# Optimization experiments

Measured on AMD Instinct MI355X. Metric: run time of the kernel, lower is better.

## Reference

```python
import jax, jax.numpy as jnp
import numpy as np

B, S, HIDDEN = 1, 2048, 3584
NH, NKV, HD = 16, 8, 256
N_REP = NH // NKV
EPS = 1e-6
SCALING = 256.0 ** -0.5  # query_pre_attn_scalar=256
SOFTCAP = 50.0
NEG = -1e9


def rmsnorm(x, w):
    # Gemma RMSNorm with unit offset, computed in fp32
    xf = x.astype(jnp.float32)
    n = xf * jax.lax.rsqrt(jnp.mean(xf * xf, axis=-1, keepdims=True) + EPS)
    return (n * (1.0 + w.astype(jnp.float32))).astype(x.dtype)


def rope(x, cos, sin):
    # x: [B,S,H,D]; gemma pairs (x[:D/2], x[D/2:]) as complex (rotate-half)
    x1, x2 = jnp.split(x, 2, axis=-1)
    c = cos[None, :, None, :]
    s = sin[None, :, None, :]
    return jnp.concatenate([x1 * c - x2 * s, x1 * s + x2 * c], axis=-1).astype(x.dtype)


def setup_inputs() -> dict:
    key = jax.random.key(0)
    ks = jax.random.split(key, 6)
    hidden_states = jax.random.normal(ks[0], (B, S, HIDDEN), jnp.float32)
    w_qkv = jax.random.normal(ks[1], ((NH + 2 * NKV) * HD, HIDDEN), jnp.float32) * 0.02
    w_o = jax.random.normal(ks[2], (HIDDEN, NH * HD), jnp.float32) * 0.02
    q_norm_w = jax.random.normal(ks[3], (HD,), jnp.float32) * 0.1
    k_norm_w = jax.random.normal(ks[4], (HD,), jnp.float32) * 0.1
    k_cache = jnp.zeros((B, S, NKV, HD), jnp.float32)
    v_cache = jnp.zeros((B, S, NKV, HD), jnp.float32)
    kv_write_indices = jnp.arange(S, dtype=jnp.int32)
    # rotary tables, theta=10000
    inv_freq = 1.0 / (10000.0 ** (np.arange(0, HD, 2, dtype=np.float32) / HD))
    t = np.arange(S, dtype=np.float32)
    freqs = np.outer(t, inv_freq)  # [S, HD/2]
    cos = jnp.asarray(np.cos(freqs), jnp.float32)
    sin = jnp.asarray(np.sin(freqs), jnp.float32)
    # causal additive mask [1,1,S,S]
    causal = np.tril(np.ones((S, S), dtype=bool))
    mask = jnp.asarray(np.where(causal, 0.0, NEG).astype(np.float32))[None, None]
    return {"hidden_states": hidden_states, "cos": cos, "sin": sin,
            "kv_write_indices": kv_write_indices, "k_cache": k_cache,
            "v_cache": v_cache, "mask": mask, "w_qkv": w_qkv, "w_o": w_o,
            "q_norm_w": q_norm_w, "k_norm_w": k_norm_w}


def reference(hidden_states, cos, sin, kv_write_indices, k_cache, v_cache,
              mask, w_qkv, w_o, q_norm_w, k_norm_w):
    qkv = jnp.einsum('bsh,oh->bso', hidden_states, w_qkv)
    q_size, kv_size = NH * HD, NKV * HD
    xq = qkv[..., :q_size].reshape(B, S, NH, HD)
    xk = qkv[..., q_size:q_size + kv_size].reshape(B, S, NKV, HD)
    xv = qkv[..., q_size + kv_size:].reshape(B, S, NKV, HD)
    xq = rmsnorm(xq, q_norm_w)
    xk = rmsnorm(xk, k_norm_w)
    xq = rope(xq, cos, sin)
    xk = rope(xk, cos, sin)
    # KV cache write (index_copy_ along dim 1)
    kc = k_cache.at[:, kv_write_indices].set(xk)
    vc = v_cache.at[:, kv_write_indices].set(xv)
    # GQA expand
    key = jnp.repeat(kc, N_REP, axis=2)   # [B,S,NH,HD]
    val = jnp.repeat(vc, N_REP, axis=2)
    q = xq.transpose(0, 2, 1, 3) * SCALING  # [B,NH,S,HD]
    k = key.transpose(0, 2, 1, 3)
    v = val.transpose(0, 2, 1, 3)
    scores = jnp.einsum('bhqd,bhkd->bhqk', q, k)
    scores = jnp.tanh(scores / SOFTCAP) * SOFTCAP  # logit softcapping
    scores = scores + mask
    p = jax.nn.softmax(scores, axis=-1)
    out = jnp.einsum('bhqk,bhkd->bhqd', p, v)
    out = out.transpose(0, 2, 1, 3).reshape(B, S, NH * HD)
    return jnp.einsum('bsd,hd->bsh', out, w_o)
```

## Files before the change

kernel.cpp:

```cpp
#include <hip/hip_runtime.h>

typedef __bf16 bf16;
typedef __bf16 bf16x4 __attribute__((ext_vector_type(4)));
typedef __bf16 bf16x8 __attribute__((ext_vector_type(8)));
typedef float f32x4 __attribute__((ext_vector_type(4)));

#define S_LEN 2048
#define HID   3584
#define NHEADS 16
#define NKVH   8
#define HDIM   256
#define QKV_O  8192
#define O_IN   4096

typedef const __attribute__((address_space(1))) void* gp_t;
typedef __attribute__((address_space(3))) void* sp_t;

__device__ __forceinline__ void async16(const void* g, void* s) {
  __builtin_amdgcn_global_load_lds((gp_t)g, (sp_t)s, 16, 0, 0);
}

__device__ __forceinline__ f32x4 mfma16(bf16x8 a, bf16x8 b, f32x4 c) {
  return __builtin_amdgcn_mfma_f32_16x16x32_bf16(a, b, c, 0, 0, 0);
}

__global__ __launch_bounds__(256) void cast_kernel(const float* __restrict__ in,
                                                   bf16* __restrict__ out, int n4) {
  int i = blockIdx.x * 256 + threadIdx.x;
  if (i >= n4) return;
  f32x4 v = ((const f32x4*)in)[i];
  bf16x4 o = { (bf16)v[0], (bf16)v[1], (bf16)v[2], (bf16)v[3] };
  ((bf16x4*)out)[i] = o;
}

__global__ __launch_bounds__(512, 2) void gemm_nt_8p(const bf16* __restrict__ A,
                                                     const bf16* __restrict__ B,
                                                     float* __restrict__ C,
                                                     int M, int N, int K) {
  __shared__ bf16 As0[256 * 64];
  __shared__ bf16 Bs0[256 * 64];
  __shared__ bf16 As1[256 * 64];
  __shared__ bf16 Bs1[256 * 64];
  int tid = threadIdx.x;
  int lane = tid & 63;
  int w = tid >> 6;
  int wm = w >> 2, wn = w & 3;
  int lid = blockIdx.x;
  int oid = (lid & 7) * 32 + (lid >> 3);
  int rect = oid >> 5, ri = oid & 31;
  int bm = (rect & 3) * 2 + (ri >> 4);
  int bn = (rect >> 2) * 16 + (ri & 15);
  int srow = tid >> 3, schunk = tid & 7;
  int gcol = (schunk ^ (srow & 7)) * 8;
  const bf16* Ag = A + (size_t)(bm * 256 + srow) * K + gcol;
  const bf16* Bg = B + (size_t)(bn * 256 + srow) * K + gcol;
  int soff = srow * 64 + schunk * 8;
  int fr = lane & 15, fq = lane >> 4;
  int c0 = ((fq) ^ (fr & 7)) * 8;
  int c1 = ((4 + fq) ^ (fr & 7)) * 8;
  const int arow = (wm * 128 + fr) * 64;
  const int brow = (wn * 64 + fr) * 64;

  f32x4 acc[8][4];
#pragma unroll
  for (int i = 0; i < 8; i++)
#pragma unroll
    for (int j = 0; j < 4; j++) { f32x4 z = {0.f, 0.f, 0.f, 0.f}; acc[i][j] = z; }
  bf16x8 a[8], b[8];

#define STG(gb, lb, kk, half) do {                                    \
    const bf16* _g = (gb) + (size_t)((half) * 128) * K + (kk);        \
    bf16* _l = (lb) + (half) * 128 * 64 + soff;                       \
    async16(_g, _l);                                                  \
    async16(_g + (size_t)64 * K, _l + 64 * 64);                       \
  } while (0)
#define LDA8(base, mg) do {                                           \
    const bf16* _p = (base) + arow + (mg) * 64 * 64;                  \
    _Pragma("unroll")                                                 \
    for (int i = 0; i < 4; i++) {                                     \
      a[i * 2 + 0] = *(const bf16x8*)(_p + i * 16 * 64 + c0);         \
      a[i * 2 + 1] = *(const bf16x8*)(_p + i * 16 * 64 + c1);         \
    }                                                                 \
  } while (0)
#define LDB4(base, jh) do {                                           \
    const bf16* _p = (base) + brow + (jh) * 32 * 64;                  \
    _Pragma("unroll")                                                 \
    for (int j = 0; j < 2; j++) {                                     \
      b[(jh) * 4 + j * 2 + 0] = *(const bf16x8*)(_p + j * 16 * 64 + c0); \
      b[(jh) * 4 + j * 2 + 1] = *(const bf16x8*)(_p + j * 16 * 64 + c1); \
    }                                                                 \
  } while (0)
#define MM16(mg, jh) do {                                             \
    __builtin_amdgcn_s_setprio(1);                                    \
    _Pragma("unroll")                                                 \
    for (int i = 0; i < 4; i++) {                                     \
      acc[(mg) * 4 + i][(jh) * 2 + 0] = mfma16(a[i * 2 + 0], b[(jh) * 4 + 0], acc[(mg) * 4 + i][(jh) * 2 + 0]); \
      acc[(mg) * 4 + i][(jh) * 2 + 0] = mfma16(a[i * 2 + 1], b[(jh) * 4 + 1], acc[(mg) * 4 + i][(jh) * 2 + 0]); \
      acc[(mg) * 4 + i][(jh) * 2 + 1] = mfma16(a[i * 2 + 0], b[(jh) * 4 + 2], acc[(mg) * 4 + i][(jh) * 2 + 1]); \
      acc[(mg) * 4 + i][(jh) * 2 + 1] = mfma16(a[i * 2 + 1], b[(jh) * 4 + 3], acc[(mg) * 4 + i][(jh) * 2 + 1]); \
    }                                                                 \
    __builtin_amdgcn_s_setprio(0);                                    \
  } while (0)
#define BAR() __builtin_amdgcn_s_barrier()
#define SBZ() __builtin_amdgcn_sched_barrier(0)
#define WAITV4() asm volatile("s_waitcnt vmcnt(4)" ::: "memory")

  const int nT = K >> 6;
  const int nIter = K >> 7;
  STG(Ag, As0, 0, 0); STG(Ag, As0, 0, 1);
  STG(Bg, Bs0, 0, 0); STG(Bg, Bs0, 0, 1);
  STG(Bg, Bs1, 64, 0); STG(Bg, Bs1, 64, 1);
  WAITV4();
  BAR(); SBZ();

  for (int t = 0; t < nIter; t++) {
    int T = 2 * t;
    int kA1 = (T + 1) * 64;
    int t2 = T + 2; if (t2 > nT - 1) t2 = nT - 1;
    int t3 = T + 3; if (t3 > nT - 1) t3 = nT - 1;
    int k2 = t2 * 64, k3 = t3 * 64;
    STG(Ag, As1, kA1, 0);
    LDA8(As0, 0); LDB4(Bs0, 0);
    MM16(0, 0); BAR();
    STG(Ag, As1, kA1, 1);
    LDB4(Bs0, 1);
    MM16(0, 1); BAR();
    STG(Bg, Bs0, k2, 0);
    LDA8(As0, 1);
    MM16(1, 0); BAR();
    STG(Bg, Bs0, k2, 1);
    MM16(1, 1); WAITV4(); BAR(); SBZ();
    STG(Ag, As0, k2, 0);
    LDA8(As1, 0); LDB4(Bs1, 0);
    MM16(0, 0); BAR();
    STG(Ag, As0, k2, 1);
    LDB4(Bs1, 1);
    MM16(0, 1); BAR();
    STG(Bg, Bs1, k3, 0);
    LDA8(As1, 1);
    MM16(1, 0); BAR();
    STG(Bg, Bs1, k3, 1);
    MM16(1, 1); WAITV4(); BAR(); SBZ();
  }
#undef STG
#undef LDA8
#undef LDB4
#undef MM16
#undef BAR
#undef SBZ
#undef WAITV4

  int row0 = bm * 256 + wm * 128 + fq * 4;
  int col0 = bn * 256 + wn * 64 + fr;
#pragma unroll
  for (int i = 0; i < 8; i++)
#pragma unroll
    for (int j = 0; j < 4; j++)
#pragma unroll
      for (int r = 0; r < 4; r++)
        C[(size_t)(row0 + i * 16 + r) * N + col0 + j * 16] = acc[i][j][r];
}

__global__ __launch_bounds__(256) void gemm_nt(const bf16* __restrict__ A, const bf16* __restrict__ B,
                                               float* __restrict__ C, int M, int N, int K) {
  __shared__ bf16 As[128 * 64];
  __shared__ bf16 Bs[128 * 64];
  int tid = threadIdx.x;
  int lane = tid & 63;
  int bm = blockIdx.y, bn = blockIdx.x;
  int w = tid >> 6, wm = w >> 1, wn = w & 1;
  int fr = lane & 15, fq = lane >> 4;
  int sr = tid >> 3;
  int sc = tid & 7;
  int cg = sc ^ (sr & 7);
  const bf16* Ag = A + (size_t)(bm * 128 + sr) * K + cg * 8;
  const bf16* Bg = B + (size_t)(bn * 128 + sr) * K + cg * 8;
  bf16* Asl = &As[sr * 64 + sc * 8];
  bf16* Bsl = &Bs[sr * 64 + sc * 8];
  const bf16* Af = &As[(wm * 64 + fr) * 64];
  const bf16* Bf = &Bs[(wn * 64 + fr) * 64];
  int fsw = fr & 7;
  int fo0 = ((fq ^ fsw) * 8);
  int fo1 = (((4 + fq) ^ fsw) * 8);
  f32x4 acc[4][4];
#pragma unroll
  for (int i = 0; i < 4; i++)
#pragma unroll
    for (int j = 0; j < 4; j++) { f32x4 z = {0.f, 0.f, 0.f, 0.f}; acc[i][j] = z; }
  for (int k0 = 0; k0 < K; k0 += 64) {
    __syncthreads();
#pragma unroll
    for (int p = 0; p < 4; p++) {
      async16(Ag + k0 + (size_t)(p * 32) * K, Asl + p * 32 * 64);
      async16(Bg + k0 + (size_t)(p * 32) * K, Bsl + p * 32 * 64);
    }
    __syncthreads();
#pragma unroll
    for (int ks = 0; ks < 2; ks++) {
      int fo = ks ? fo1 : fo0;
      bf16x8 a[4], b[4];
#pragma unroll
      for (int t = 0; t < 4; t++) a[t] = *(const bf16x8*)(Af + t * 16 * 64 + fo);
#pragma unroll
      for (int t = 0; t < 4; t++) b[t] = *(const bf16x8*)(Bf + t * 16 * 64 + fo);
#pragma unroll
      for (int i = 0; i < 4; i++)
#pragma unroll
        for (int j = 0; j < 4; j++) acc[i][j] = mfma16(a[i], b[j], acc[i][j]);
    }
  }
  int row0 = bm * 128 + wm * 64 + fq * 4;
  int col0 = bn * 128 + wn * 64 + fr;
#pragma unroll
  for (int i = 0; i < 4; i++)
#pragma unroll
    for (int j = 0; j < 4; j++)
#pragma unroll
      for (int r = 0; r < 4; r++)
        C[(size_t)(row0 + i * 16 + r) * N + col0 + j * 16] = acc[i][j][r];
}

__global__ __launch_bounds__(256) void qk_norm_rope(const float* __restrict__ qkv,
                                                    const float* __restrict__ cosb,
                                                    const float* __restrict__ sinb,
                                                    const float* __restrict__ qw,
                                                    const float* __restrict__ kw,
                                                    bf16* __restrict__ qout,
                                                    bf16* __restrict__ kout) {
  int s = blockIdx.x;
  int lane = threadIdx.x & 63;
  int w = threadIdx.x >> 6;
  int d0 = lane * 4;
  int dr = d0 & 127;
  f32x4 cv = *(const f32x4*)(cosb + s * 128 + dr);
  f32x4 sv = *(const f32x4*)(sinb + s * 128 + dr);
  bool hi = lane >= 32;
#pragma unroll
  for (int r = 0; r < 6; r++) {
    int head = r * 4 + w;
    const float* x = qkv + (size_t)s * QKV_O + head * HDIM + d0;
    f32x4 v = *(const f32x4*)x;
    float ss = v[0] * v[0] + v[1] * v[1] + v[2] * v[2] + v[3] * v[3];
#pragma unroll
    for (int off = 32; off > 0; off >>= 1) ss += __shfl_xor(ss, off);
    float scale = rsqrtf(ss * (1.0f / HDIM) + 1e-6f);
    bool isq = head < NHEADS;
    const float* wn = isq ? qw : kw;
    f32x4 wv = *(const f32x4*)(wn + d0);
    float y[4], o[4];
#pragma unroll
    for (int i = 0; i < 4; i++) y[i] = v[i] * scale * (1.0f + wv[i]);
#pragma unroll
    for (int i = 0; i < 4; i++) {
      float py = __shfl_xor(y[i], 32);
      o[i] = hi ? (py * sv[i] + y[i] * cv[i]) : (y[i] * cv[i] - py * sv[i]);
    }
    float mult = isq ? 0.0625f : 1.0f;
    bf16x4 ov = { (bf16)(o[0] * mult), (bf16)(o[1] * mult), (bf16)(o[2] * mult), (bf16)(o[3] * mult) };
    if (isq) *(bf16x4*)(qout + ((size_t)head * S_LEN + s) * HDIM + d0) = ov;
    else     *(bf16x4*)(kout + ((size_t)(head - NHEADS) * S_LEN + s) * HDIM + d0) = ov;
  }
}

__global__ __launch_bounds__(256) void v_transpose(const float* __restrict__ qkv, bf16* __restrict__ vt) {
  __shared__ float tile[64][65];
  int dt = blockIdx.x, st = blockIdx.y, h = blockIdx.z;
  int t = threadIdx.x;
  int d0 = dt * 64, s0 = st * 64;
#pragma unroll
  for (int i = 0; i < 16; i++) {
    int idx = i * 256 + t;
    int r = idx >> 6, c = idx & 63;
    tile[r][c] = qkv[(size_t)(s0 + r) * QKV_O + 6144 + h * HDIM + d0 + c];
  }
  __syncthreads();
#pragma unroll
  for (int i = 0; i < 16; i++) {
    int idx = i * 256 + t;
    int dr = idx >> 6, sc = idx & 63;
    vt[((size_t)h * HDIM + d0 + dr) * S_LEN + s0 + sc] = (bf16)tile[sc][dr];
  }
}

#define PSTRIDE 40
__global__ __launch_bounds__(256) void attn_kernel(const bf16* __restrict__ q,
                                                   const bf16* __restrict__ kx,
                                                   const bf16* __restrict__ vt,
                                                   bf16* __restrict__ aout) {
  __shared__ bf16 kt[32 * 256];
  __shared__ bf16 vtile[256 * 32];
  __shared__ bf16 pbuf[4][16 * PSTRIDE];
  int h = blockIdx.x;
  int y = blockIdx.y;
  int qt = (y < 16) ? y : 47 - y;
  int kvh = h >> 1;
  int tid = threadIdx.x;
  int lane = tid & 63, w = tid >> 6;
  int fr = lane & 15, fq = lane >> 4;
  int qs = qt * 64;
  bf16x8 qf[8];
  const bf16* qb = q + ((size_t)h * S_LEN + qs + w * 16 + fr) * HDIM + fq * 8;
#pragma unroll
  for (int i = 0; i < 8; i++) qf[i] = *(const bf16x8*)(qb + i * 32);
  f32x4 acc[16];
#pragma unroll
  for (int i = 0; i < 16; i++) { f32x4 z = {0.f, 0.f, 0.f, 0.f}; acc[i] = z; }
  float lsum[4] = {0.f, 0.f, 0.f, 0.f};
  int krow = w * 2 + (lane >> 5);
  int kcolr = (lane & 31) * 8;
  const bf16* kg = kx + (size_t)kvh * S_LEN * HDIM;
  int vd = w * 16 + (lane >> 2);
  int vsw = (vd >> 1) & 3;
  int vcl = (lane & 3) * 8;
  int vcg = (((lane & 3) ^ vsw) * 8);
  const bf16* vg = vt + (size_t)kvh * HDIM * S_LEN;
  int rot0 = (fq * 8 - fr * 8) & 255;
  int rot1 = (fq * 8 - fr * 8 - 128) & 255;
  const bf16* kt0 = &kt[fr * 256];
  const bf16* kt1 = &kt[(16 + fr) * 256];
  int fsw = (fr >> 1) & 3;
  int kmax = qs + 64;
  for (int k0 = 0; k0 < kmax; k0 += 32) {
    __syncthreads();
#pragma unroll
    for (int p = 0; p < 4; p++) {
      int r = p * 8 + krow;
      int gc = (kcolr + r * 8) & 255;
      async16(kg + (size_t)(k0 + r) * HDIM + gc, &kt[r * 256 + kcolr]);
      int d = p * 64 + vd;
      async16(vg + (size_t)d * S_LEN + k0 + vcg, &vtile[d * 32 + vcl]);
    }
    __syncthreads();
    f32x4 s0 = {0.f, 0.f, 0.f, 0.f}, s1 = {0.f, 0.f, 0.f, 0.f};
#pragma unroll
    for (int kk = 0; kk < 8; kk++) {
      bf16x8 b0 = *(const bf16x8*)(kt0 + ((kk * 32 + rot0) & 255));
      bf16x8 b1 = *(const bf16x8*)(kt1 + ((kk * 32 + rot1) & 255));
      s0 = mfma16(qf[kk], b0, s0);
      s1 = mfma16(qf[kk], b1, s1);
    }
#pragma unroll
    for (int reg = 0; reg < 4; reg++) {
      int rowg = qs + w * 16 + fq * 4 + reg;
      float u0 = __builtin_amdgcn_exp2f(0.057707802f * s0[reg]);
      float u1 = __builtin_amdgcn_exp2f(0.057707802f * s1[reg]);
      float p0 = __builtin_amdgcn_exp2f(28.853901f - 144.26950f * __builtin_amdgcn_rcpf(u0 + 1.0f));
      float p1 = __builtin_amdgcn_exp2f(28.853901f - 144.26950f * __builtin_amdgcn_rcpf(u1 + 1.0f));
      p0 = (k0 + fr <= rowg) ? p0 : 0.0f;
      p1 = (k0 + 16 + fr <= rowg) ? p1 : 0.0f;
      lsum[reg] += p0 + p1;
      pbuf[w][(fq * 4 + reg) * PSTRIDE + fr] = (bf16)p0;
      pbuf[w][(fq * 4 + reg) * PSTRIDE + 16 + fr] = (bf16)p1;
    }
    bf16x8 pf = *(const bf16x8*)&pbuf[w][fr * PSTRIDE + fq * 8];
#pragma unroll
    for (int ct = 0; ct < 16; ct++) {
      bf16x8 vf = *(const bf16x8*)&vtile[(ct * 16 + fr) * 32 + (fq ^ fsw) * 8];
      acc[ct] = mfma16(pf, vf, acc[ct]);
    }
  }
  float rl[4];
#pragma unroll
  for (int reg = 0; reg < 4; reg++) {
    float l = lsum[reg];
    l += __shfl_xor(l, 1);
    l += __shfl_xor(l, 2);
    l += __shfl_xor(l, 4);
    l += __shfl_xor(l, 8);
    rl[reg] = 1.0f / l;
  }
#pragma unroll
  for (int ct = 0; ct < 16; ct++)
#pragma unroll
    for (int reg = 0; reg < 4; reg++)
      aout[(size_t)(qs + w * 16 + fq * 4 + reg) * O_IN + h * HDIM + ct * 16 + fr] =
          (bf16)(acc[ct][reg] * rl[reg]);
}

extern "C" void kernel_launch(void* const* d_in, const int* in_sizes, int n_in,
                              void* d_out, int out_size, void* d_ws, size_t ws_size,
                              hipStream_t stream) {
  const float* hidden = (const float*)d_in[0];
  const float* cosb   = (const float*)d_in[1];
  const float* sinb   = (const float*)d_in[2];
  const float* wqkv   = (const float*)d_in[7];
  const float* wo     = (const float*)d_in[8];
  const float* qnw    = (const float*)d_in[9];
  const float* knw    = (const float*)d_in[10];
  float* out = (float*)d_out;
  char* ws = (char*)d_ws;
  bf16*  h_bf    = (bf16*)(ws + 0);
  bf16*  wqkv_bf = (bf16*)(ws + 14680064);
  bf16*  wo_bf   = (bf16*)(ws + 73400320);
  float* qkv     = (float*)(ws + 102760448);
  bf16*  qb      = (bf16*)(ws + 169869312);
  bf16*  kb      = (bf16*)(ws + 186646528);
  bf16*  vtb     = (bf16*)(ws + 195035136);
  bf16*  attnb   = (bf16*)(ws + 203423744);

  cast_kernel<<<7168, 256, 0, stream>>>(hidden, h_bf, 1835008);
  cast_kernel<<<28672, 256, 0, stream>>>(wqkv, wqkv_bf, 7340032);
  cast_kernel<<<14336, 256, 0, stream>>>(wo, wo_bf, 3670016);
  gemm_nt_8p<<<256, 512, 0, stream>>>(h_bf, wqkv_bf, qkv, 2048, 8192, 3584);
  qk_norm_rope<<<2048, 256, 0, stream>>>(qkv, cosb, sinb, qnw, knw, qb, kb);
  v_transpose<<<dim3(4, 32, 8), 256, 0, stream>>>(qkv, vtb);
  attn_kernel<<<dim3(16, 32), 256, 0, stream>>>(qb, kb, vtb, attnb);
  gemm_nt<<<dim3(28, 16), 256, 0, stream>>>(attnb, wo_bf, out, 2048, 3584, 4096);
}
```

Baseline: 598.9 us.

## Replace output projection GEMM with pipelined 256x256 split-K kernel plus reduction

The output projection previously used a simple 128x128 tile GEMM. It now uses the larger double-buffered, 8-wave 256x256 tile pipeline, split into two K halves across 224 blocks. The two partial results go into workspace and are summed by a separate add kernel. This is meant to improve MFMA utilisation and CU occupancy, at the cost of writing and re-reading two fp32 partial outputs and launching one more kernel.

```diff
diff --git a/kernel.cpp b/kernel.cpp
--- a/kernel.cpp
+++ b/kernel.cpp
@@ -31,6 +31,16 @@
   f32x4 v = ((const f32x4*)in)[i];
   bf16x4 o = { (bf16)v[0], (bf16)v[1], (bf16)v[2], (bf16)v[3] };
   ((bf16x4*)out)[i] = o;
+}
+
+__global__ __launch_bounds__(256) void add2_kernel(const float* __restrict__ a,
+                                                   const float* __restrict__ b,
+                                                   float* __restrict__ o, int n4) {
+  int i = blockIdx.x * 256 + threadIdx.x;
+  if (i >= n4) return;
+  f32x4 x = ((const f32x4*)a)[i];
+  f32x4 y = ((const f32x4*)b)[i];
+  ((f32x4*)o)[i] = x + y;
 }
 
 __global__ __launch_bounds__(512, 2) void gemm_nt_8p(const bf16* __restrict__ A,
@@ -161,63 +171,135 @@
         C[(size_t)(row0 + i * 16 + r) * N + col0 + j * 16] = acc[i][j][r];
 }
 
-__global__ __launch_bounds__(256) void gemm_nt(const bf16* __restrict__ A, const bf16* __restrict__ B,
-                                               float* __restrict__ C, int M, int N, int K) {
-  __shared__ bf16 As[128 * 64];
-  __shared__ bf16 Bs[128 * 64];
+__global__ __launch_bounds__(512, 2) void gemm_nt_8p_ks(const bf16* __restrict__ A,
+                                                        const bf16* __restrict__ B,
+                                                        float* __restrict__ C,
+                                                        int M, int N, int K, int lda) {
+  __shared__ bf16 As0[256 * 64];
+  __shared__ bf16 Bs0[256 * 64];
+  __shared__ bf16 As1[256 * 64];
+  __shared__ bf16 Bs1[256 * 64];
   int tid = threadIdx.x;
   int lane = tid & 63;
-  int bm = blockIdx.y, bn = blockIdx.x;
-  int w = tid >> 6, wm = w >> 1, wn = w & 1;
+  int w = tid >> 6;
+  int wm = w >> 2, wn = w & 3;
+  int lid = blockIdx.x;
+  int ks = lid >= 112;
+  int l2 = lid - ks * 112;
+  int oid = (l2 & 7) * 14 + (l2 >> 3);
+  int bm = oid / 14;
+  int bn = oid - bm * 14;
+  int kbase = ks * K;
+  float* Cp = C + (size_t)ks * M * N;
+  int srow = tid >> 3, schunk = tid & 7;
+  int gcol = (schunk ^ (srow & 7)) * 8;
+  const bf16* Ag = A + (size_t)(bm * 256 + srow) * lda + kbase + gcol;
+  const bf16* Bg = B + (size_t)(bn * 256 + srow) * lda + kbase + gcol;
+  int soff = srow * 64 + schunk * 8;
   int fr = lane & 15, fq = lane >> 4;
-  int sr = tid >> 3;
-  int sc = tid & 7;
-  int cg = sc ^ (sr & 7);
-  const bf16* Ag = A + (size_t)(bm * 128 + sr) * K + cg * 8;
-  const bf16* Bg = B + (size_t)(bn * 128 + sr) * K + cg * 8;
-  bf16* Asl = &As[sr * 64 + sc * 8];
-  bf16* Bsl = &Bs[sr * 64 + sc * 8];
-  const bf16* Af = &As[(wm * 64 + fr) * 64];
-  const bf16* Bf = &Bs[(wn * 64 + fr) * 64];
-  int fsw = fr & 7;
-  int fo0 = ((fq ^ fsw) * 8);
-  int fo1 = (((4 + fq) ^ fsw) * 8);
-  f32x4 acc[4][4];
-#pragma unroll
-  for (int i = 0; i < 4; i++)
+  int c0 = ((fq) ^ (fr & 7)) * 8;
+  int c1 = ((4 + fq) ^ (fr & 7)) * 8;
+  const int arow = (wm * 128 + fr) * 64;
+  const int brow = (wn * 64 + fr) * 64;
+
+  f32x4 acc[8][4];
+#pragma unroll
+  for (int i = 0; i < 8; i++)
 #pragma unroll
     for (int j = 0; j < 4; j++) { f32x4 z = {0.f, 0.f, 0.f, 0.f}; acc[i][j] = z; }
-  for (int k0 = 0; k0 < K; k0 += 64) {
-    __syncthreads();
-#pragma unroll
-    for (int p = 0; p < 4; p++) {
-      async16(Ag + k0 + (size_t)(p * 32) * K, Asl + p * 32 * 64);
-      async16(Bg + k0 + (size_t)(p * 32) * K, Bsl + p * 32 * 64);
-    }
-    __syncthreads();
-#pragma unroll
-    for (int ks = 0; ks < 2; ks++) {
-      int fo = ks ? fo1 : fo0;
-      bf16x8 a[4], b[4];
-#pragma unroll
-      for (int t = 0; t < 4; t++) a[t] = *(const bf16x8*)(Af + t * 16 * 64 + fo);
-#pragma unroll
-      for (int t = 0; t < 4; t++) b[t] = *(const bf16x8*)(Bf + t * 16 * 64 + fo);
-#pragma unroll
-      for (int i = 0; i < 4; i++)
-#pragma unroll
-        for (int j = 0; j < 4; j++) acc[i][j] = mfma16(a[i], b[j], acc[i][j]);
-    }
-  }
-  int row0 = bm * 128 + wm * 64 + fq * 4;
-  int col0 = bn * 128 + wn * 64 + fr;
-#pragma unroll
-  for (int i = 0; i < 4; i++)
+  bf16x8 a[8], b[8];
+
+#define STG(gb, lb, kk, half) do {                                    \
+    const bf16* _g = (gb) + (size_t)((half) * 128) * lda + (kk);      \
+    bf16* _l = (lb) + (half) * 128 * 64 + soff;                       \
+    async16(_g, _l);                                                  \
+    async16(_g + (size_t)64 * lda, _l + 64 * 64);                     \
+  } while (0)
+#define LDA8(base, mg) do {                                           \
+    const bf16* _p = (base) + arow + (mg) * 64 * 64;                  \
+    _Pragma("unroll")                                                 \
+    for (int i = 0; i < 4; i++) {                                     \
+      a[i * 2 + 0] = *(const bf16x8*)(_p + i * 16 * 64 + c0);         \
+      a[i * 2 + 1] = *(const bf16x8*)(_p + i * 16 * 64 + c1);         \
+    }                                                                 \
+  } while (0)
+#define LDB4(base, jh) do {                                           \
+    const bf16* _p = (base) + brow + (jh) * 32 * 64;                  \
+    _Pragma("unroll")                                                 \
+    for (int j = 0; j < 2; j++) {                                     \
+      b[(jh) * 4 + j * 2 + 0] = *(const bf16x8*)(_p + j * 16 * 64 + c0); \
+      b[(jh) * 4 + j * 2 + 1] = *(const bf16x8*)(_p + j * 16 * 64 + c1); \
+    }                                                                 \
+  } while (0)
+#define MM16(mg, jh) do {                                             \
+    __builtin_amdgcn_s_setprio(1);                                    \
+    _Pragma("unroll")                                                 \
+    for (int i = 0; i < 4; i++) {                                     \
+      acc[(mg) * 4 + i][(jh) * 2 + 0] = mfma16(a[i * 2 + 0], b[(jh) * 4 + 0], acc[(mg) * 4 + i][(jh) * 2 + 0]); \
+      acc[(mg) * 4 + i][(jh) * 2 + 0] = mfma16(a[i * 2 + 1], b[(jh) * 4 + 1], acc[(mg) * 4 + i][(jh) * 2 + 0]); \
+      acc[(mg) * 4 + i][(jh) * 2 + 1] = mfma16(a[i * 2 + 0], b[(jh) * 4 + 2], acc[(mg) * 4 + i][(jh) * 2 + 1]); \
+      acc[(mg) * 4 + i][(jh) * 2 + 1] = mfma16(a[i * 2 + 1], b[(jh) * 4 + 3], acc[(mg) * 4 + i][(jh) * 2 + 1]); \
+    }                                                                 \
+    __builtin_amdgcn_s_setprio(0);                                    \
+  } while (0)
+#define BAR() __builtin_amdgcn_s_barrier()
+#define SBZ() __builtin_amdgcn_sched_barrier(0)
+#define WAITV4() asm volatile("s_waitcnt vmcnt(4)" ::: "memory")
+
+  const int nT = K >> 6;
+  const int nIter = K >> 7;
+  STG(Ag, As0, 0, 0); STG(Ag, As0, 0, 1);
+  STG(Bg, Bs0, 0, 0); STG(Bg, Bs0, 0, 1);
+  STG(Bg, Bs1, 64, 0); STG(Bg, Bs1, 64, 1);
+  WAITV4();
+  BAR(); SBZ();
+
+  for (int t = 0; t < nIter; t++) {
+    int T = 2 * t;
+    int kA1 = (T + 1) * 64;
+    int t2 = T + 2; if (t2 > nT - 1) t2 = nT - 1;
+    int t3 = T + 3; if (t3 > nT - 1) t3 = nT - 1;
+    int k2 = t2 * 64, k3 = t3 * 64;
+    STG(Ag, As1, kA1, 0);
+    LDA8(As0, 0); LDB4(Bs0, 0);
+    MM16(0, 0); BAR();
+    STG(Ag, As1, kA1, 1);
+    LDB4(Bs0, 1);
+    MM16(0, 1); BAR();
+    STG(Bg, Bs0, k2, 0);
+    LDA8(As0, 1);
+    MM16(1, 0); BAR();
+    STG(Bg, Bs0, k2, 1);
+    MM16(1, 1); WAITV4(); BAR(); SBZ();
+    STG(Ag, As0, k2, 0);
+    LDA8(As1, 0); LDB4(Bs1, 0);
+    MM16(0, 0); BAR();
+    STG(Ag, As0, k2, 1);
+    LDB4(Bs1, 1);
+    MM16(0, 1); BAR();
+    STG(Bg, Bs1, k3, 0);
+    LDA8(As1, 1);
+    MM16(1, 0); BAR();
+    STG(Bg, Bs1, k3, 1);
+    MM16(1, 1); WAITV4(); BAR(); SBZ();
+  }
+#undef STG
+#undef LDA8
+#undef LDB4
+#undef MM16
+#undef BAR
+#undef SBZ
+#undef WAITV4
+
+  int row0 = bm * 256 + wm * 128 + fq * 4;
+  int col0 = bn * 256 + wn * 64 + fr;
+#pragma unroll
+  for (int i = 0; i < 8; i++)
 #pragma unroll
     for (int j = 0; j < 4; j++)
 #pragma unroll
       for (int r = 0; r < 4; r++)
-        C[(size_t)(row0 + i * 16 + r) * N + col0 + j * 16] = acc[i][j][r];
+        Cp[(size_t)(row0 + i * 16 + r) * N + col0 + j * 16] = acc[i][j][r];
 }
 
 __global__ __launch_bounds__(256) void qk_norm_rope(const float* __restrict__ qkv,
@@ -397,6 +479,8 @@
   bf16*  kb      = (bf16*)(ws + 186646528);
   bf16*  vtb     = (bf16*)(ws + 195035136);
   bf16*  attnb   = (bf16*)(ws + 203423744);
+  float* part0   = (float*)(ws + 102760448);
+  float* part1   = part0 + (size_t)2048 * 3584;
 
   cast_kernel<<<7168, 256, 0, stream>>>(hidden, h_bf, 1835008);
   cast_kernel<<<28672, 256, 0, stream>>>(wqkv, wqkv_bf, 7340032);
@@ -405,5 +489,6 @@
   qk_norm_rope<<<2048, 256, 0, stream>>>(qkv, cosb, sinb, qnw, knw, qb, kb);
   v_transpose<<<dim3(4, 32, 8), 256, 0, stream>>>(qkv, vtb);
   attn_kernel<<<dim3(16, 32), 256, 0, stream>>>(qb, kb, vtb, attnb);
-  gemm_nt<<<dim3(28, 16), 256, 0, stream>>>(attnb, wo_bf, out, 2048, 3584, 4096);
-}
+  gemm_nt_8p_ks<<<224, 512, 0, stream>>>(attnb, wo_bf, part0, 2048, 3584, 2048, 4096);
+  add2_kernel<<<7168, 256, 0, stream>>>(part0, part1, out, 1835008);
+}
```

New measurement: 604.4 us. About the same (+0.9%).
